# Optimization experiments

Hardware: AMD Instinct MI355X
Metric: run time of the kernel (lower is better)

Reference implementation:

```python
import jax, jax.numpy as jnp
import numpy as np
from jax import lax

THRE = 0.01
K_SIZE = 5
C_SIGMA = 1.0
VOXEL = 0.4          # args['voxel_size'][0] -> discrete_ratio
DOWNSAMPLE = 4       # args['downsample_rate']


def gaussian_kernel(k=K_SIZE, sigma=C_SIGMA):
    c = k // 2
    gx, gy = np.mgrid[-c:k - c, -c:k - c]
    g = 1.0 / (2.0 * np.pi * sigma) * np.exp(-(gx ** 2 + gy ** 2) / (2.0 * sigma ** 2))
    return jnp.asarray(g, dtype=jnp.float32)


def affine_grid(theta, H, W):
    # theta: [N,2,3]; matches F.affine_grid(align_corners=False)
    dt = theta.dtype
    xs = (jnp.arange(W, dtype=dt) + 0.5) * (2.0 / W) - 1.0
    ys = (jnp.arange(H, dtype=dt) + 0.5) * (2.0 / H) - 1.0
    xg, yg = jnp.meshgrid(xs, ys)                      # [H,W]
    base = jnp.stack([xg, yg, jnp.ones_like(xg)], -1)  # [H,W,3]
    return jnp.einsum('hwk,nck->nhwc', base, theta)    # [N,H,W,2] (x_s, y_s)


def grid_sample_bilinear(src, grid):
    # src [N,C,H,W], grid [N,H,W,2] in [-1,1]; bilinear, zeros padding, align_corners=False
    N, C, H, W = src.shape
    x = ((grid[..., 0] + 1.0) * W - 1.0) * 0.5
    y = ((grid[..., 1] + 1.0) * H - 1.0) * 0.5
    x0f = jnp.floor(x)
    y0f = jnp.floor(y)
    wx1 = x - x0f
    wy1 = y - y0f

    def sample_one(src_n, x0f_n, y0f_n, wx1_n, wy1_n):
        x0 = x0f_n.astype(jnp.int32)
        y0 = y0f_n.astype(jnp.int32)

        def gather(ix, iy):
            valid = ((ix >= 0) & (ix < W) & (iy >= 0) & (iy < H)).astype(src.dtype)
            ixc = jnp.clip(ix, 0, W - 1)
            iyc = jnp.clip(iy, 0, H - 1)
            return src_n[:, iyc, ixc] * valid[None]    # [C,H,W]

        g00 = gather(x0, y0)
        g01 = gather(x0 + 1, y0)
        g10 = gather(x0, y0 + 1)
        g11 = gather(x0 + 1, y0 + 1)
        wx0 = 1.0 - wx1_n
        wy0 = 1.0 - wy1_n
        return (g00 * (wx0 * wy0)[None] + g01 * (wx1_n * wy0)[None]
                + g10 * (wx0 * wy1_n)[None] + g11 * (wx1_n * wy1_n)[None])

    return jax.vmap(sample_one)(src, x0f, y0f, wx1, wy1)


def atten_fuse(feat):
    # feat: [N,C,H,W]; per-pixel scaled-dot-product attention over agents, keep ego row.
    N, C, H, W = feat.shape
    seq = feat.reshape(N, C, H * W).transpose(2, 0, 1)          # [HW, N, C]
    q0 = seq[:, 0, :]                                           # ego query [HW, C]
    score = jnp.einsum('pc,pnc->pn', q0, seq) / np.sqrt(C)      # row 0 of NxN scores
    attn = jax.nn.softmax(score, axis=-1)
    ctx = jnp.einsum('pn,pnc->pc', attn, seq)                   # [HW, C]
    return ctx.T.reshape(C, H, W)


def _forward(x, psm_single, pairwise_t_matrix):
    B, L = pairwise_t_matrix.shape[:2]
    _, C, H, W = x.shape
    A = psm_single.shape[1]

    # ---- normalize 4x4 transforms to 2x3 affine matrices (as in Where2comm.forward)
    t = pairwise_t_matrix[..., :2, :][..., jnp.array([0, 1, 3])]   # [B,L,L,2,3]
    t = t.at[..., 0, 1].multiply(H / W)
    t = t.at[..., 1, 0].multiply(W / H)
    t = t.at[..., 0, 2].set(t[..., 0, 2] / (DOWNSAMPLE * VOXEL * W) * 2.0)
    t = t.at[..., 1, 2].set(t[..., 1, 2] / (DOWNSAMPLE * VOXEL * H) * 2.0)

    # ---- Communication: confidence -> gaussian smooth -> threshold mask
    conf = jnp.max(jax.nn.sigmoid(psm_single), axis=1, keepdims=True)  # [B*L,1,H,W]
    gk = gaussian_kernel()
    pad = (K_SIZE - 1) // 2
    smoothed = lax.conv_general_dilated(
        conf, gk[None, None], (1, 1), [(pad, pad), (pad, pad)],
        dimension_numbers=('NCHW', 'OIHW', 'NCHW'))
    mask = (smoothed > THRE).astype(x.dtype)                            # [B*L,1,H,W]
    mask = mask.reshape(B, L, 1, H, W)
    mask = mask.at[:, ::2].set(1.0)                                     # nodiag trick per batch
    rate = jnp.mean(jnp.sum(mask[:, 0], axis=(1, 2, 3)) / (H * W))

    # ---- mask features, warp every agent into ego frame, attention-fuse
    xm = x.reshape(B, L, C, H, W) * mask[:, :, :, :, :]                 # broadcast over C

    def fuse_scene(feat_b, t_b):
        # feat_b: [L,C,H,W]; t_b: [L,L,2,3]; ego row of transforms warps all agents to ego
        grid = affine_grid(t_b[0], H, W)                                # [L,H,W,2]
        neighbor = grid_sample_bilinear(feat_b, grid)                   # [L,C,H,W]
        return atten_fuse(neighbor)                                     # [C,H,W]

    x_fuse = jax.vmap(fuse_scene)(xm, t)                                # [B,C,H,W]
    return x_fuse, rate


def setup_inputs() -> dict:
    key = jax.random.key(0)
    B, L, C, A, H, W = 2, 5, 256, 2, 100, 252
    k1, k2, k3 = jax.random.split(key, 3)
    x = jax.random.normal(k1, (B * L, C, H, W), jnp.float32)
    psm_single = jax.random.normal(k2, (B * L, A, H, W), jnp.float32)
    # near-identity 4x4 pose transforms with small random translations (meters)
    t = jnp.tile(jnp.eye(4, dtype=jnp.float32), (B, L, L, 1, 1))
    trans = jax.random.uniform(k3, (B, L, L, 2), jnp.float32, -10.0, 10.0)
    t = t.at[..., 0, 3].set(trans[..., 0])
    t = t.at[..., 1, 3].set(trans[..., 1])
    idx = jnp.arange(L)
    t = t.at[:, idx, idx].set(jnp.eye(4, dtype=jnp.float32))  # self-transform = identity
    record_len = jnp.full((B,), L, dtype=jnp.int32)
    return {"x": x, "psm_single": psm_single, "pairwise_t_matrix": t, "record_len": record_len}


def reference(x, psm_single, pairwise_t_matrix, record_len):
    x_fuse, rate = _forward(x, psm_single, pairwise_t_matrix)
    return x_fuse
```

## Files before the change

### kernel.cpp

```cpp
#include <hip/hip_runtime.h>
#include <math.h>

#define BB 2
#define LL 5
#define CC 256
#define HH 100
#define WW 252
#define HW (HH*WW)
#define CHW (CC*HW)
#define THRE_F 0.01f

__device__ const float GW[5][5] = {
    {0.002915024f, 0.013064233f, 0.021539279f, 0.013064233f, 0.002915024f},
    {0.013064233f, 0.058549832f, 0.096532353f, 0.058549832f, 0.013064233f},
    {0.021539279f, 0.096532353f, 0.159154943f, 0.096532353f, 0.021539279f},
    {0.013064233f, 0.058549832f, 0.096532353f, 0.058549832f, 0.013064233f},
    {0.002915024f, 0.013064233f, 0.021539279f, 0.013064233f, 0.002915024f},
};

__device__ __forceinline__ float2 ld2(const float* p) {
    float2 v;
    __builtin_memcpy(&v, p, sizeof(float2));
    return v;
}

__global__ void mask_kernel(const float* __restrict__ psm, float* __restrict__ mask)
{
    int idx = blockIdx.x * blockDim.x + threadIdx.x;
    if (idx >= 4 * HW) return;
    int m = idx / HW;
    int p = idx - m * HW;
    int h = p / WW;
    int w = p - h * WW;
    int n = (m >> 1) * LL + ((m & 1) * 2 + 1);
    const float* base0 = psm + (size_t)n * 2 * HW;
    const float* base1 = base0 + HW;

    float acc = 0.0f;
#pragma unroll
    for (int i = 0; i < 5; ++i) {
        int yy = h + i - 2;
        if (yy < 0 || yy >= HH) continue;
#pragma unroll
        for (int j = 0; j < 5; ++j) {
            int xx = w + j - 2;
            if (xx < 0 || xx >= WW) continue;
            float v = fmaxf(base0[yy * WW + xx], base1[yy * WW + xx]);
            acc += GW[i][j] / (1.0f + __expf(-v));
        }
    }
    mask[idx] = (acc > THRE_F) ? 1.0f : 0.0f;
}

struct TapSetup {
    int   off0[LL], off1[LL];
    float a0[LL], b0[LL], a1[LL], b1[LL];
};

__device__ __forceinline__ void make_taps(
    int b, int h, int w, bool active, int c0,
    const float* __restrict__ pt, const float* __restrict__ mask, TapSetup& T)
{
    float xsn = (w + 0.5f) * (2.0f / WW) - 1.0f;
    float ysn = (h + 0.5f) * (2.0f / HH) - 1.0f;
    float act = active ? 1.0f : 0.0f;

#pragma unroll
    for (int l = 0; l < LL; ++l) {
        const float* M = pt + (size_t)(b * LL * LL + l) * 16;
        float t00 = M[0];
        float t01 = M[1] * (100.0f / 252.0f);
        float t02 = M[3] / 403.2f * 2.0f;
        float t10 = M[4] * (252.0f / 100.0f);
        float t11 = M[5];
        float t12 = M[7] / 160.0f * 2.0f;

        float gx = t00 * xsn + t01 * ysn + t02;
        float gy = t10 * xsn + t11 * ysn + t12;
        float fx = ((gx + 1.0f) * WW - 1.0f) * 0.5f;
        float fy = ((gy + 1.0f) * HH - 1.0f) * 0.5f;
        float fx0 = floorf(fx), fy0 = floorf(fy);
        float wx1 = fx - fx0,  wy1 = fy - fy0;
        float wx0 = 1.0f - wx1, wy0 = 1.0f - wy1;
        int x0 = (int)fx0, y0 = (int)fy0;
        int x1 = x0 + 1,   y1 = y0 + 1;

        int cx0 = min(max(x0, 0), WW - 1), cx1 = min(max(x1, 0), WW - 1);
        int cy0 = min(max(y0, 0), HH - 1), cy1 = min(max(y1, 0), HH - 1);

        float vx0 = (x0 >= 0 && x0 < WW) ? 1.0f : 0.0f;
        float vx1 = (x1 >= 0 && x1 < WW) ? 1.0f : 0.0f;
        float vy0 = (y0 >= 0 && y0 < HH) ? 1.0f : 0.0f;
        float vy1 = (y1 >= 0 && y1 < HH) ? 1.0f : 0.0f;

        float m00 = 1.0f, m01 = 1.0f, m10 = 1.0f, m11 = 1.0f;
        if (l & 1) {
            const float* mb = mask + (size_t)(b * 2 + (l >> 1)) * HW;
            m00 = mb[cy0 * WW + cx0];
            m01 = mb[cy0 * WW + cx1];
            m10 = mb[cy1 * WW + cx0];
            m11 = mb[cy1 * WW + cx1];
        }

        float w00 = wx0 * wy0 * vx0 * vy0 * m00 * act;
        float w01 = wx1 * wy0 * vx1 * vy0 * m01 * act;
        float w10 = wx0 * wy1 * vx0 * vy1 * m10 * act;
        float w11 = wx1 * wy1 * vx1 * vy1 * m11 * act;

        int bx = min(max(x0, 0), WW - 2);
        int d  = x0 - bx;
        T.a0[l] = (d == 0 ? w00 : 0.0f) + (d == -1 ? w01 : 0.0f);
        T.b0[l] = (d == 0 ? w01 : 0.0f) + (d ==  1 ? w00 : 0.0f);
        T.a1[l] = (d == 0 ? w10 : 0.0f) + (d == -1 ? w11 : 0.0f);
        T.b1[l] = (d == 0 ? w11 : 0.0f) + (d ==  1 ? w10 : 0.0f);

        int nbase = (b * LL + l) * CHW + c0 * HW;
        T.off0[l] = nbase + cy0 * WW + bx;
        T.off1[l] = nbase + cy1 * WW + bx;
    }
}

__global__ __launch_bounds__(256) void score_kernel(
    const float* __restrict__ x, const float* __restrict__ pt,
    const float* __restrict__ mask, float* __restrict__ scoresP)
{
    int blk = blockIdx.x;
    int cc = blk & 1;
    int t  = blk >> 1;
    int wt = t & 3; t >>= 2;
    int h  = t % HH;
    int b  = t / HH;

    int tid = threadIdx.x;
    int wl  = tid & 63;
    int cg  = tid >> 6;
    int w   = wt * 64 + wl;
    bool active = (w < WW);
    int c0 = cc * 128 + cg * 32;

    TapSetup T;
    make_taps(b, h, w, active, c0, pt, mask, T);

    float s[LL] = {0.f, 0.f, 0.f, 0.f, 0.f};
    for (int i = 0; i < 32; ++i) {
        float2 r0[LL], r1[LL];
#pragma unroll
        for (int l = 0; l < LL; ++l) {
            r0[l] = ld2(x + T.off0[l]);
            r1[l] = ld2(x + T.off1[l]);
        }
        float f0 = T.a0[0] * r0[0].x + T.b0[0] * r0[0].y
                 + T.a1[0] * r1[0].x + T.b1[0] * r1[0].y;
        s[0] += f0 * f0;
#pragma unroll
        for (int l = 1; l < LL; ++l) {
            float fl = T.a0[l] * r0[l].x + T.b0[l] * r0[l].y
                     + T.a1[l] * r1[l].x + T.b1[l] * r1[l].y;
            s[l] += f0 * fl;
        }
#pragma unroll
        for (int l = 0; l < LL; ++l) { T.off0[l] += HW; T.off1[l] += HW; }
    }

    __shared__ float sred[4][LL][64];
#pragma unroll
    for (int l = 0; l < LL; ++l) sred[cg][l][wl] = s[l];
    __syncthreads();

    if (tid < 64 && active) {
        int p = h * WW + w;
#pragma unroll
        for (int l = 0; l < LL; ++l) {
            float v = sred[0][l][wl] + sred[1][l][wl]
                    + sred[2][l][wl] + sred[3][l][wl];
            scoresP[((cc * BB + b) * LL + l) * HW + p] = v;
        }
    }
}

__global__ __launch_bounds__(256) void out_kernel(
    const float* __restrict__ x, const float* __restrict__ pt,
    const float* __restrict__ mask, const float* __restrict__ scoresP,
    float* __restrict__ out)
{
    int blk = blockIdx.x;
    int cc = blk & 1;
    int t  = blk >> 1;
    int wt = t & 3; t >>= 2;
    int h  = t % HH;
    int b  = t / HH;

    int tid = threadIdx.x;
    int wl  = tid & 63;
    int cg  = tid >> 6;
    int w   = wt * 64 + wl;
    bool active = (w < WW);
    int c0 = cc * 128 + cg * 32;

    float a[LL];
    if (active) {
        int p = h * WW + w;
        float mx = -1e30f;
#pragma unroll
        for (int l = 0; l < LL; ++l) {
            float v = (scoresP[(b * LL + l) * HW + p]
                     + scoresP[((BB + b) * LL + l) * HW + p]) * 0.0625f;
            a[l] = v;
            mx = fmaxf(mx, v);
        }
        float denom = 0.0f;
#pragma unroll
        for (int l = 0; l < LL; ++l) { a[l] = expf(a[l] - mx); denom += a[l]; }
        float inv = 1.0f / denom;
#pragma unroll
        for (int l = 0; l < LL; ++l) a[l] *= inv;
    } else {
#pragma unroll
        for (int l = 0; l < LL; ++l) a[l] = 0.0f;
    }

    TapSetup T;
    make_taps(b, h, w, active, c0, pt, mask, T);
#pragma unroll
    for (int l = 0; l < LL; ++l) {
        T.a0[l] *= a[l]; T.b0[l] *= a[l]; T.a1[l] *= a[l]; T.b1[l] *= a[l];
    }

    int obase = b * CHW + c0 * HW + h * WW + w;
    for (int i = 0; i < 32; ++i) {
        float2 r0[LL], r1[LL];
#pragma unroll
        for (int l = 0; l < LL; ++l) {
            r0[l] = ld2(x + T.off0[l]);
            r1[l] = ld2(x + T.off1[l]);
        }
        float ctx = 0.0f;
#pragma unroll
        for (int l = 0; l < LL; ++l) {
            ctx += T.a0[l] * r0[l].x + T.b0[l] * r0[l].y
                 + T.a1[l] * r1[l].x + T.b1[l] * r1[l].y;
        }
        if (active) out[obase + i * HW] = ctx;
#pragma unroll
        for (int l = 0; l < LL; ++l) { T.off0[l] += HW; T.off1[l] += HW; }
    }
}

extern "C" void kernel_launch(void* const* d_in, const int* in_sizes, int n_in,
                              void* d_out, int out_size, void* d_ws, size_t ws_size,
                              hipStream_t stream)
{
    const float* x   = (const float*)d_in[0];
    const float* psm = (const float*)d_in[1];
    const float* pt  = (const float*)d_in[2];
    float* out = (float*)d_out;

    float* maskw  = (float*)d_ws;
    float* scores = maskw + 4 * HW;

    mask_kernel<<<(4 * HW + 255) / 256, 256, 0, stream>>>(psm, maskw);
    score_kernel<<<BB * HH * 4 * 2, 256, 0, stream>>>(x, pt, maskw, scores);
    out_kernel<<<BB * HH * 4 * 2, 256, 0, stream>>>(x, pt, maskw, scores, out);
}
```

Measured before the change: 512.6 us.

## Process two pixels per thread with a vectorized translation-only fast path

Each thread now handles two adjacent pixels and the grid is halved. A runtime check detects when all pose transforms are pure translations; in that case the bilinear taps share one fractional offset, so the kernel loads aligned 4-float windows per row and applies precomputed 16-coefficient dot products. The generic affine path stays as a fallback. It also moves the 1/16 score scaling into the score kernel and uses __expf, aiming to cut gather instruction count and address setup at the cost of more registers and code size.

New measurement: 501.6 us. 2.1% less time.

```diff
diff --git a/kernel.cpp b/kernel.cpp
--- a/kernel.cpp
+++ b/kernel.cpp
@@ -10,6 +10,23 @@
 #define CHW (CC*HW)
 #define THRE_F 0.01f
 
+typedef float v2f __attribute__((ext_vector_type(2)));
+typedef float v4f __attribute__((ext_vector_type(4)));
+
+__device__ __forceinline__ v2f ld2v(const float* p) {
+    v2f v; __builtin_memcpy(&v, p, 8); return v;
+}
+__device__ __forceinline__ v4f ld4v(const float* p) {
+    v4f v; __builtin_memcpy(&v, p, 16); return v;
+}
+__device__ __forceinline__ void st2v(float* p, v2f v) {
+    __builtin_memcpy(p, &v, 8);
+}
+__device__ __forceinline__ float dot8(const float* c, v4f A, v4f B) {
+    return c[0]*A.x + c[1]*A.y + c[2]*A.z + c[3]*A.w
+         + c[4]*B.x + c[5]*B.y + c[6]*B.z + c[7]*B.w;
+}
+
 __device__ const float GW[5][5] = {
     {0.002915024f, 0.013064233f, 0.021539279f, 0.013064233f, 0.002915024f},
     {0.013064233f, 0.058549832f, 0.096532353f, 0.058549832f, 0.013064233f},
@@ -17,12 +34,6 @@
     {0.013064233f, 0.058549832f, 0.096532353f, 0.058549832f, 0.013064233f},
     {0.002915024f, 0.013064233f, 0.021539279f, 0.013064233f, 0.002915024f},
 };
-
-__device__ __forceinline__ float2 ld2(const float* p) {
-    float2 v;
-    __builtin_memcpy(&v, p, sizeof(float2));
-    return v;
-}
 
 __global__ void mask_kernel(const float* __restrict__ psm, float* __restrict__ mask)
 {
@@ -52,197 +63,333 @@
     mask[idx] = (acc > THRE_F) ? 1.0f : 0.0f;
 }
 
-struct TapSetup {
-    int   off0[LL], off1[LL];
-    float a0[LL], b0[LL], a1[LL], b1[LL];
-};
-
-__device__ __forceinline__ void make_taps(
-    int b, int h, int w, bool active, int c0,
-    const float* __restrict__ pt, const float* __restrict__ mask, TapSetup& T)
-{
-    float xsn = (w + 0.5f) * (2.0f / WW) - 1.0f;
+struct XF { float t00, t01, t02, t10, t11, t12; };
+
+__device__ __forceinline__ XF load_xf(const float* __restrict__ pt, int b, int l) {
+    const float* M = pt + (size_t)(b * LL * LL + l) * 16;
+    XF X;
+    X.t00 = M[0];
+    X.t01 = M[1] * (100.0f / 252.0f);
+    X.t02 = M[3] / 403.2f * 2.0f;
+    X.t10 = M[4] * (252.0f / 100.0f);
+    X.t11 = M[5];
+    X.t12 = M[7] / 160.0f * 2.0f;
+    return X;
+}
+__device__ __forceinline__ bool is_trans(const XF& X) {
+    return X.t00 == 1.0f && X.t01 == 0.0f && X.t10 == 0.0f && X.t11 == 1.0f;
+}
+
+__device__ __forceinline__ void setup_trans(
+    int l, int b, int h, int px0, float act, const XF& X,
+    const float* __restrict__ maskw, int cstart,
+    float cf[16], int o2[2])
+{
+    float tx = X.t02 * (WW * 0.5f);
+    float ty = X.t12 * (HH * 0.5f);
+    int ix = (int)floorf(tx);
+    int iy = (int)floorf(ty);
+    float wx1 = tx - (float)ix, wx0 = 1.0f - wx1;
+    float wy1 = ty - (float)iy, wy0 = 1.0f - wy1;
+    int y0 = h + iy, y1 = y0 + 1;
+    int cy0 = min(max(y0, 0), HH - 1), cy1 = min(max(y1, 0), HH - 1);
+    float vy0 = (y0 >= 0 && y0 < HH) ? 1.0f : 0.0f;
+    float vy1 = (y1 >= 0 && y1 < HH) ? 1.0f : 0.0f;
+
+    int craw = px0 + ix;
+    int col = craw & ~1;
+    col = min(max(col, 0), WW - 4);
+    int d = craw - col;
+
+    const float* mb = nullptr;
+    if (l & 1) mb = maskw + (size_t)(b * 2 + (l >> 1)) * HW;
+
+#pragma unroll
+    for (int k = 0; k < 16; ++k) cf[k] = 0.0f;
+#pragma unroll
+    for (int px = 0; px < 2; ++px) {
+#pragma unroll
+        for (int r = 0; r < 2; ++r) {
+#pragma unroll
+            for (int t = 0; t < 2; ++t) {
+                int xt = craw + px + t;
+                float vx  = (xt >= 0 && xt < WW) ? 1.0f : 0.0f;
+                float wcol = t ? wx1 : wx0;
+                float wrow = r ? wy1 : wy0;
+                float vyw  = r ? vy1 : vy0;
+                float m = 1.0f;
+                if (mb) {
+                    int cx = min(max(xt, 0), WW - 1);
+                    int cy = r ? cy1 : cy0;
+                    m = mb[cy * WW + cx];
+                }
+                float wgt = wcol * wrow * vyw * vx * m * act;
+                int e = d + px + t;
+#pragma unroll
+                for (int k = 0; k < 4; ++k)
+                    if (e == k) cf[px * 8 + r * 4 + k] += wgt;
+            }
+        }
+    }
+    int nbase = (b * LL + l) * CHW + cstart * HW;
+    o2[0] = nbase + cy0 * WW + col;
+    o2[1] = nbase + cy1 * WW + col;
+}
+
+__device__ __forceinline__ void setup_gen(
+    int l, int b, int h, int px0, float act, const XF& X,
+    const float* __restrict__ maskw, int cstart,
+    float gc[8], int o4[4])
+{
+    const float* mb = nullptr;
+    if (l & 1) mb = maskw + (size_t)(b * 2 + (l >> 1)) * HW;
     float ysn = (h + 0.5f) * (2.0f / HH) - 1.0f;
-    float act = active ? 1.0f : 0.0f;
-
-#pragma unroll
-    for (int l = 0; l < LL; ++l) {
-        const float* M = pt + (size_t)(b * LL * LL + l) * 16;
-        float t00 = M[0];
-        float t01 = M[1] * (100.0f / 252.0f);
-        float t02 = M[3] / 403.2f * 2.0f;
-        float t10 = M[4] * (252.0f / 100.0f);
-        float t11 = M[5];
-        float t12 = M[7] / 160.0f * 2.0f;
-
-        float gx = t00 * xsn + t01 * ysn + t02;
-        float gy = t10 * xsn + t11 * ysn + t12;
+    int nbase = (b * LL + l) * CHW + cstart * HW;
+
+#pragma unroll
+    for (int px = 0; px < 2; ++px) {
+        float xsn = (px0 + px + 0.5f) * (2.0f / WW) - 1.0f;
+        float gx = X.t00 * xsn + X.t01 * ysn + X.t02;
+        float gy = X.t10 * xsn + X.t11 * ysn + X.t12;
         float fx = ((gx + 1.0f) * WW - 1.0f) * 0.5f;
         float fy = ((gy + 1.0f) * HH - 1.0f) * 0.5f;
         float fx0 = floorf(fx), fy0 = floorf(fy);
-        float wx1 = fx - fx0,  wy1 = fy - fy0;
+        float wx1 = fx - fx0, wy1 = fy - fy0;
         float wx0 = 1.0f - wx1, wy0 = 1.0f - wy1;
         int x0 = (int)fx0, y0 = (int)fy0;
-        int x1 = x0 + 1,   y1 = y0 + 1;
-
+        int x1 = x0 + 1, y1 = y0 + 1;
         int cx0 = min(max(x0, 0), WW - 1), cx1 = min(max(x1, 0), WW - 1);
         int cy0 = min(max(y0, 0), HH - 1), cy1 = min(max(y1, 0), HH - 1);
-
         float vx0 = (x0 >= 0 && x0 < WW) ? 1.0f : 0.0f;
         float vx1 = (x1 >= 0 && x1 < WW) ? 1.0f : 0.0f;
         float vy0 = (y0 >= 0 && y0 < HH) ? 1.0f : 0.0f;
         float vy1 = (y1 >= 0 && y1 < HH) ? 1.0f : 0.0f;
-
-        float m00 = 1.0f, m01 = 1.0f, m10 = 1.0f, m11 = 1.0f;
-        if (l & 1) {
-            const float* mb = mask + (size_t)(b * 2 + (l >> 1)) * HW;
-            m00 = mb[cy0 * WW + cx0];
-            m01 = mb[cy0 * WW + cx1];
-            m10 = mb[cy1 * WW + cx0];
-            m11 = mb[cy1 * WW + cx1];
-        }
-
+        float m00 = 1, m01 = 1, m10 = 1, m11 = 1;
+        if (mb) {
+            m00 = mb[cy0 * WW + cx0]; m01 = mb[cy0 * WW + cx1];
+            m10 = mb[cy1 * WW + cx0]; m11 = mb[cy1 * WW + cx1];
+        }
         float w00 = wx0 * wy0 * vx0 * vy0 * m00 * act;
         float w01 = wx1 * wy0 * vx1 * vy0 * m01 * act;
         float w10 = wx0 * wy1 * vx0 * vy1 * m10 * act;
         float w11 = wx1 * wy1 * vx1 * vy1 * m11 * act;
-
         int bx = min(max(x0, 0), WW - 2);
-        int d  = x0 - bx;
-        T.a0[l] = (d == 0 ? w00 : 0.0f) + (d == -1 ? w01 : 0.0f);
-        T.b0[l] = (d == 0 ? w01 : 0.0f) + (d ==  1 ? w00 : 0.0f);
-        T.a1[l] = (d == 0 ? w10 : 0.0f) + (d == -1 ? w11 : 0.0f);
-        T.b1[l] = (d == 0 ? w11 : 0.0f) + (d ==  1 ? w10 : 0.0f);
-
-        int nbase = (b * LL + l) * CHW + c0 * HW;
-        T.off0[l] = nbase + cy0 * WW + bx;
-        T.off1[l] = nbase + cy1 * WW + bx;
+        int dd = x0 - bx;
+        gc[px * 4 + 0] = (dd == 0 ? w00 : 0.f) + (dd == -1 ? w01 : 0.f);
+        gc[px * 4 + 1] = (dd == 0 ? w01 : 0.f) + (dd ==  1 ? w00 : 0.f);
+        gc[px * 4 + 2] = (dd == 0 ? w10 : 0.f) + (dd == -1 ? w11 : 0.f);
+        gc[px * 4 + 3] = (dd == 0 ? w11 : 0.f) + (dd ==  1 ? w10 : 0.f);
+        o4[px * 2 + 0] = nbase + cy0 * WW + bx;
+        o4[px * 2 + 1] = nbase + cy1 * WW + bx;
     }
 }
 
 __global__ __launch_bounds__(256) void score_kernel(
     const float* __restrict__ x, const float* __restrict__ pt,
-    const float* __restrict__ mask, float* __restrict__ scoresP)
+    const float* __restrict__ maskw, float* __restrict__ scoresP)
 {
     int blk = blockIdx.x;
     int cc = blk & 1;
-    int t  = blk >> 1;
-    int wt = t & 3; t >>= 2;
+    int wt = (blk >> 1) & 1;
+    int t  = blk >> 2;
     int h  = t % HH;
     int b  = t / HH;
 
     int tid = threadIdx.x;
-    int wl  = tid & 63;
-    int cg  = tid >> 6;
-    int w   = wt * 64 + wl;
-    bool active = (w < WW);
-    int c0 = cc * 128 + cg * 32;
-
-    TapSetup T;
-    make_taps(b, h, w, active, c0, pt, mask, T);
-
-    float s[LL] = {0.f, 0.f, 0.f, 0.f, 0.f};
-    for (int i = 0; i < 32; ++i) {
-        float2 r0[LL], r1[LL];
+    int lane = tid & 63;
+    int cg   = tid >> 6;
+    int px0  = wt * 128 + 2 * lane;
+    float act = (px0 < WW) ? 1.0f : 0.0f;
+    v2f act2 = {act, act};
+    int cstart = cc * 128 + cg * 32;
+
+    XF X[LL];
+#pragma unroll
+    for (int l = 0; l < LL; ++l) X[l] = load_xf(pt, b, l);
+    bool ident0 = is_trans(X[0]) && X[0].t02 == 0.0f && X[0].t12 == 0.0f;
+    bool ftrans = ident0 && is_trans(X[1]) && is_trans(X[2])
+                         && is_trans(X[3]) && is_trans(X[4]);
+
+    v2f s[LL];
+#pragma unroll
+    for (int l = 0; l < LL; ++l) s[l] = (v2f){0.f, 0.f};
+
+    if (ftrans) {
+        int f0off = b * LL * CHW + cstart * HW + h * WW + min(px0, WW - 2);
+        float cf[4][16];
+        int o[8];
+#pragma unroll
+        for (int l = 1; l < LL; ++l)
+            setup_trans(l, b, h, px0, act, X[l], maskw, cstart, cf[l - 1], &o[(l - 1) * 2]);
+
+        for (int ci = 0; ci < 32; ++ci) {
+            v2f f0 = ld2v(x + f0off) * act2;  f0off += HW;
+            s[0] += f0 * f0;
+#pragma unroll
+            for (int l = 1; l < LL; ++l) {
+                v4f F0 = ld4v(x + o[(l - 1) * 2 + 0]);
+                v4f F1 = ld4v(x + o[(l - 1) * 2 + 1]);
+                o[(l - 1) * 2 + 0] += HW;
+                o[(l - 1) * 2 + 1] += HW;
+                v2f fl;
+                fl.x = dot8(&cf[l - 1][0], F0, F1);
+                fl.y = dot8(&cf[l - 1][8], F0, F1);
+                s[l] += f0 * fl;
+            }
+        }
+    } else {
+        float gc[LL][8];
+        int go[LL][4];
+#pragma unroll
+        for (int l = 0; l < LL; ++l)
+            setup_gen(l, b, h, px0, act, X[l], maskw, cstart, gc[l], go[l]);
+
+        for (int ci = 0; ci < 32; ++ci) {
+            v2f fv[LL];
+#pragma unroll
+            for (int l = 0; l < LL; ++l) {
+                v2f R00 = ld2v(x + go[l][0]);
+                v2f R01 = ld2v(x + go[l][1]);
+                v2f R10 = ld2v(x + go[l][2]);
+                v2f R11 = ld2v(x + go[l][3]);
+#pragma unroll
+                for (int k = 0; k < 4; ++k) go[l][k] += HW;
+                fv[l].x = gc[l][0]*R00.x + gc[l][1]*R00.y + gc[l][2]*R01.x + gc[l][3]*R01.y;
+                fv[l].y = gc[l][4]*R10.x + gc[l][5]*R10.y + gc[l][6]*R11.x + gc[l][7]*R11.y;
+            }
+#pragma unroll
+            for (int l = 0; l < LL; ++l) s[l] += fv[0] * fv[l];
+        }
+    }
+
+    __shared__ v2f sred[4][LL][64];
+#pragma unroll
+    for (int l = 0; l < LL; ++l) sred[cg][l][lane] = s[l];
+    __syncthreads();
+
+    if (tid < 64 && px0 < WW) {
+        int p = h * WW + px0;
 #pragma unroll
         for (int l = 0; l < LL; ++l) {
-            r0[l] = ld2(x + T.off0[l]);
-            r1[l] = ld2(x + T.off1[l]);
-        }
-        float f0 = T.a0[0] * r0[0].x + T.b0[0] * r0[0].y
-                 + T.a1[0] * r1[0].x + T.b1[0] * r1[0].y;
-        s[0] += f0 * f0;
-#pragma unroll
-        for (int l = 1; l < LL; ++l) {
-            float fl = T.a0[l] * r0[l].x + T.b0[l] * r0[l].y
-                     + T.a1[l] * r1[l].x + T.b1[l] * r1[l].y;
-            s[l] += f0 * fl;
-        }
-#pragma unroll
-        for (int l = 0; l < LL; ++l) { T.off0[l] += HW; T.off1[l] += HW; }
-    }
-
-    __shared__ float sred[4][LL][64];
-#pragma unroll
-    for (int l = 0; l < LL; ++l) sred[cg][l][wl] = s[l];
-    __syncthreads();
-
-    if (tid < 64 && active) {
-        int p = h * WW + w;
-#pragma unroll
-        for (int l = 0; l < LL; ++l) {
-            float v = sred[0][l][wl] + sred[1][l][wl]
-                    + sred[2][l][wl] + sred[3][l][wl];
-            scoresP[((cc * BB + b) * LL + l) * HW + p] = v;
+            v2f v = (sred[0][l][lane] + sred[1][l][lane]
+                   + sred[2][l][lane] + sred[3][l][lane]) * 0.0625f;
+            st2v(&scoresP[((cc * BB + b) * LL + l) * HW + p], v);
         }
     }
 }
 
 __global__ __launch_bounds__(256) void out_kernel(
     const float* __restrict__ x, const float* __restrict__ pt,
-    const float* __restrict__ mask, const float* __restrict__ scoresP,
+    const float* __restrict__ maskw, const float* __restrict__ scoresP,
     float* __restrict__ out)
 {
     int blk = blockIdx.x;
     int cc = blk & 1;
-    int t  = blk >> 1;
-    int wt = t & 3; t >>= 2;
+    int wt = (blk >> 1) & 1;
+    int t  = blk >> 2;
     int h  = t % HH;
     int b  = t / HH;
 
     int tid = threadIdx.x;
-    int wl  = tid & 63;
-    int cg  = tid >> 6;
-    int w   = wt * 64 + wl;
-    bool active = (w < WW);
-    int c0 = cc * 128 + cg * 32;
-
-    float a[LL];
-    if (active) {
-        int p = h * WW + w;
-        float mx = -1e30f;
+    int lane = tid & 63;
+    int cg   = tid >> 6;
+    int px0  = wt * 128 + 2 * lane;
+    float act = (px0 < WW) ? 1.0f : 0.0f;
+    v2f act2 = {act, act};
+    int cstart = cc * 128 + cg * 32;
+
+    v2f a[LL];
+    {
+        int p = min(h * WW + px0, HW - 2);
+        v2f mx = {-1e30f, -1e30f};
 #pragma unroll
         for (int l = 0; l < LL; ++l) {
-            float v = (scoresP[(b * LL + l) * HW + p]
-                     + scoresP[((BB + b) * LL + l) * HW + p]) * 0.0625f;
-            a[l] = v;
-            mx = fmaxf(mx, v);
-        }
-        float denom = 0.0f;
-#pragma unroll
-        for (int l = 0; l < LL; ++l) { a[l] = expf(a[l] - mx); denom += a[l]; }
-        float inv = 1.0f / denom;
+            v2f sc = ld2v(scoresP + (b * LL + l) * HW + p)
+                   + ld2v(scoresP + ((BB + b) * LL + l) * HW + p);
+            a[l] = sc;
+            mx.x = fmaxf(mx.x, sc.x);
+            mx.y = fmaxf(mx.y, sc.y);
+        }
+        v2f denom = {0.f, 0.f};
+#pragma unroll
+        for (int l = 0; l < LL; ++l) {
+            a[l].x = __expf(a[l].x - mx.x);
+            a[l].y = __expf(a[l].y - mx.y);
+            denom += a[l];
+        }
+        v2f inv = {1.0f / denom.x, 1.0f / denom.y};
 #pragma unroll
         for (int l = 0; l < LL; ++l) a[l] *= inv;
+    }
+
+    XF X[LL];
+#pragma unroll
+    for (int l = 0; l < LL; ++l) X[l] = load_xf(pt, b, l);
+    bool ident0 = is_trans(X[0]) && X[0].t02 == 0.0f && X[0].t12 == 0.0f;
+    bool ftrans = ident0 && is_trans(X[1]) && is_trans(X[2])
+                         && is_trans(X[3]) && is_trans(X[4]);
+
+    int obase = b * CHW + cstart * HW + h * WW + px0;
+    bool doStore = (px0 < WW);
+
+    if (ftrans) {
+        int f0off = b * LL * CHW + cstart * HW + h * WW + min(px0, WW - 2);
+        float cf[4][16];
+        int o[8];
+#pragma unroll
+        for (int l = 1; l < LL; ++l) {
+            setup_trans(l, b, h, px0, act, X[l], maskw, cstart, cf[l - 1], &o[(l - 1) * 2]);
+#pragma unroll
+            for (int k = 0; k < 8; ++k) {
+                cf[l - 1][k]     *= a[l].x;
+                cf[l - 1][k + 8] *= a[l].y;
+            }
+        }
+        v2f af0 = a[0] * act2;
+
+        for (int ci = 0; ci < 32; ++ci) {
+            v2f f0 = ld2v(x + f0off);  f0off += HW;
+            v2f ctx = af0 * f0;
+#pragma unroll
+            for (int l = 1; l < LL; ++l) {
+                v4f F0 = ld4v(x + o[(l - 1) * 2 + 0]);
+                v4f F1 = ld4v(x + o[(l - 1) * 2 + 1]);
+                o[(l - 1) * 2 + 0] += HW;
+                o[(l - 1) * 2 + 1] += HW;
+                ctx.x += dot8(&cf[l - 1][0], F0, F1);
+                ctx.y += dot8(&cf[l - 1][8], F0, F1);
+            }
+            if (doStore) st2v(&out[obase], ctx);
+            obase += HW;
+        }
     } else {
-#pragma unroll
-        for (int l = 0; l < LL; ++l) a[l] = 0.0f;
-    }
-
-    TapSetup T;
-    make_taps(b, h, w, active, c0, pt, mask, T);
-#pragma unroll
-    for (int l = 0; l < LL; ++l) {
-        T.a0[l] *= a[l]; T.b0[l] *= a[l]; T.a1[l] *= a[l]; T.b1[l] *= a[l];
-    }
-
-    int obase = b * CHW + c0 * HW + h * WW + w;
-    for (int i = 0; i < 32; ++i) {
-        float2 r0[LL], r1[LL];
+        float gc[LL][8];
+        int go[LL][4];
 #pragma unroll
         for (int l = 0; l < LL; ++l) {
-            r0[l] = ld2(x + T.off0[l]);
-            r1[l] = ld2(x + T.off1[l]);
-        }
-        float ctx = 0.0f;
-#pragma unroll
-        for (int l = 0; l < LL; ++l) {
-            ctx += T.a0[l] * r0[l].x + T.b0[l] * r0[l].y
-                 + T.a1[l] * r1[l].x + T.b1[l] * r1[l].y;
-        }
-        if (active) out[obase + i * HW] = ctx;
-#pragma unroll
-        for (int l = 0; l < LL; ++l) { T.off0[l] += HW; T.off1[l] += HW; }
+            setup_gen(l, b, h, px0, act, X[l], maskw, cstart, gc[l], go[l]);
+#pragma unroll
+            for (int k = 0; k < 4; ++k) {
+                gc[l][k]     *= a[l].x;
+                gc[l][k + 4] *= a[l].y;
+            }
+        }
+        for (int ci = 0; ci < 32; ++ci) {
+            v2f ctx = {0.f, 0.f};
+#pragma unroll
+            for (int l = 0; l < LL; ++l) {
+                v2f R00 = ld2v(x + go[l][0]);
+                v2f R01 = ld2v(x + go[l][1]);
+                v2f R10 = ld2v(x + go[l][2]);
+                v2f R11 = ld2v(x + go[l][3]);
+#pragma unroll
+                for (int k = 0; k < 4; ++k) go[l][k] += HW;
+                ctx.x += gc[l][0]*R00.x + gc[l][1]*R00.y + gc[l][2]*R01.x + gc[l][3]*R01.y;
+                ctx.y += gc[l][4]*R10.x + gc[l][5]*R10.y + gc[l][6]*R11.x + gc[l][7]*R11.y;
+            }
+            if (doStore) st2v(&out[obase], ctx);
+            obase += HW;
+        }
     }
 }
 
@@ -259,6 +406,6 @@
     float* scores = maskw + 4 * HW;
 
     mask_kernel<<<(4 * HW + 255) / 256, 256, 0, stream>>>(psm, maskw);
-    score_kernel<<<BB * HH * 4 * 2, 256, 0, stream>>>(x, pt, maskw, scores);
-    out_kernel<<<BB * HH * 4 * 2, 256, 0, stream>>>(x, pt, maskw, scores, out);
-}
+    score_kernel<<<BB * HH * 2 * 2, 256, 0, stream>>>(x, pt, maskw, scores);
+    out_kernel<<<BB * HH * 2 * 2, 256, 0, stream>>>(x, pt, maskw, scores, out);
+}
```
